# Performance work log

Hardware: AMD Instinct MI355X
Metric: run time of the kernel (lower is better)

Reference implementation:

```python
import jax, jax.numpy as jnp
import numpy as np

EPS = 1e-5

def _layernorm(x, g, b):
    m = jnp.mean(x, axis=-1, keepdims=True)
    v = jnp.mean((x - m) ** 2, axis=-1, keepdims=True)
    return (x - m) * jax.lax.rsqrt(v + EPS) * g + b

def setup_inputs() -> dict:
    key = jax.random.key(0)
    ks = jax.random.split(key, 16)
    B, N, L, E, D, NL = 1, 40962, 256, 4, 163848, 6
    inp = {}
    inp['mesh_latent'] = jax.random.normal(ks[0], (B, N, L), dtype=jnp.float32)
    inp['edge_index'] = jax.random.randint(ks[1], (2, D), 0, N, dtype=jnp.int32)
    inp['edge_attr'] = jax.random.normal(ks[2], (D, E), dtype=jnp.float32)
    s_e = 1.0 / np.sqrt(2 * L + E)
    s_n = 1.0 / np.sqrt(2 * L)
    s_o = 1.0 / np.sqrt(L)
    inp['We_w'] = jax.random.uniform(ks[3], (NL, 2 * L + E, L), jnp.float32, -s_e, s_e)
    inp['We_b'] = jax.random.uniform(ks[4], (NL, L), jnp.float32, -s_e, s_e)
    inp['ln1_g'] = jnp.ones((NL, L), jnp.float32)
    inp['ln1_b'] = jnp.zeros((NL, L), jnp.float32)
    inp['Wn1_w'] = jax.random.uniform(ks[5], (NL, 2 * L, L), jnp.float32, -s_n, s_n)
    inp['Wn1_b'] = jax.random.uniform(ks[6], (NL, L), jnp.float32, -s_n, s_n)
    inp['ln2_g'] = jnp.ones((NL, L), jnp.float32)
    inp['ln2_b'] = jnp.zeros((NL, L), jnp.float32)
    inp['Wn2_w'] = jax.random.uniform(ks[7], (NL, L, L), jnp.float32, -s_o, s_o)
    inp['Wn2_b'] = jax.random.uniform(ks[8], (NL, L), jnp.float32, -s_o, s_o)
    return inp

def reference(mesh_latent, edge_index, edge_attr, We_w, We_b, ln1_g, ln1_b,
              Wn1_w, Wn1_b, ln2_g, ln2_b, Wn2_w, Wn2_b):
    src = edge_index[0]  # x_j (source)
    dst = edge_index[1]  # x_i (target), also aggregation index
    N = mesh_latent.shape[1]
    L = mesh_latent.shape[2]
    # precompute edge_attr contribution is layer-dependent, done inside scan

    def layer(x, p):
        we_w, we_b, g1, b1, wn1_w, wn1_b, g2, b2, wn2_w, wn2_b = p
        x_i = x[dst]  # [E, L] target node feats
        x_j = x[src]  # [E, L] source node feats
        # edge MLP on cat([x_i, x_j, edge_attr]) without materializing the concat
        h = x_i @ we_w[:L] + x_j @ we_w[L:2 * L] + edge_attr @ we_w[2 * L:] + we_b
        msg = jax.nn.silu(_layernorm(h, g1, b1))  # [E, L]
        agg = jax.ops.segment_sum(msg, dst, num_segments=N)  # [N, L]
        u = x @ wn1_w[:L] + agg @ wn1_w[L:] + wn1_b
        u = jax.nn.silu(_layernorm(u, g2, b2)) @ wn2_w + wn2_b
        return x + u, None

    params = (We_w, We_b, ln1_g, ln1_b, Wn1_w, Wn1_b, ln2_g, ln2_b, Wn2_w, Wn2_b)

    def per_sample(x):
        x_out, _ = jax.lax.scan(layer, x, params)
        return x_out

    return jax.vmap(per_sample)(mesh_latent)
```

## Files before the change

### kernel.cpp

```cpp
#include <hip/hip_runtime.h>
#include <hip/hip_bf16.h>
#include <math.h>


#define NNODES 40962
#define NEDGES 163848
#define NLAYERS 6
#define MPAD 41088

typedef __attribute__((ext_vector_type(8))) short short8;
typedef __attribute__((ext_vector_type(4))) float f32x4;
typedef unsigned short ushort_t;

__device__ __forceinline__ void async_copy16(void* lds, const void* g) {
    __builtin_amdgcn_global_load_lds(
        (const __attribute__((address_space(1))) unsigned int*)g,
        (__attribute__((address_space(3))) unsigned int*)lds, 16, 0, 0);
}

__device__ __forceinline__ void bsplit(float v, ushort_t& h, ushort_t& l) {
    unsigned int u = __float_as_uint(v);
    h = (ushort_t)(u >> 16);
    float hf = __uint_as_float(u & 0xFFFF0000u);
    l = (ushort_t)(__float_as_uint(v - hf) >> 16);
}

__global__ __launch_bounds__(256) void wprep_kernel(
    const float* __restrict__ src, ushort_t* __restrict__ dst,
    int R, int C, size_t src_lstride, size_t src_hstride, int halves)
{
    __shared__ float t[32][33];
    const int b = blockIdx.z;
    src += (size_t)(b / halves) * src_lstride + (size_t)(b % halves) * src_hstride;
    dst += (size_t)b * R * C;
    const int tx = threadIdx.x & 31, ty = threadIdx.x >> 5;
    const int c0 = blockIdx.x * 32, r0 = blockIdx.y * 32;
    #pragma unroll
    for (int i = 0; i < 4; ++i)
        t[ty + 8 * i][tx] = src[(size_t)(r0 + ty + 8 * i) * C + c0 + tx];
    __syncthreads();
    #pragma unroll
    for (int i = 0; i < 4; ++i) {
        unsigned int u = __float_as_uint(t[tx][ty + 8 * i]);
        ushort_t h = (ushort_t)((u + 0x7FFFu + ((u >> 16) & 1u)) >> 16);
        dst[(size_t)(c0 + ty + 8 * i) * R + r0 + tx] = h;
    }
}

__global__ __launch_bounds__(256) void split_kernel(
    const float* __restrict__ x, ushort_t* __restrict__ xh,
    ushort_t* __restrict__ xl, int n4)
{
    int idx = blockIdx.x * 256 + threadIdx.x;
    if (idx >= n4) return;
    float4 v = ((const float4*)x)[idx];
    ushort4 oh, ol;
    bsplit(v.x, oh.x, ol.x); bsplit(v.y, oh.y, ol.y);
    bsplit(v.z, oh.z, ol.z); bsplit(v.w, oh.w, ol.w);
    ((ushort4*)xh)[idx] = oh;
    ((ushort4*)xl)[idx] = ol;
}

__global__ __launch_bounds__(256) void gemm_mfma(
    const ushort_t* __restrict__ A1h, const ushort_t* __restrict__ A1l,
    const ushort_t* __restrict__ A2h, const ushort_t* __restrict__ A2l,
    const ushort_t* __restrict__ BT,
    const float* __restrict__ bias, const float* __restrict__ resid,
    float* __restrict__ C, ushort_t* __restrict__ Ch, ushort_t* __restrict__ Cl,
    int M, int K, int ldC)
{
    __shared__ __align__(16) short AhS[128 * 32];
    __shared__ __align__(16) short AlS[128 * 32];
    __shared__ __align__(16) short BsS[128 * 32];

    const int tid = threadIdx.x;
    const int wave = tid >> 6;
    const int lane = tid & 63;
    const int m0 = blockIdx.x * 128;
    const int n0 = blockIdx.y * 128;
    const int wm = wave >> 1, wn = wave & 1;
    const int fm = lane & 15, quad = lane >> 4;

    const int rA = wave * 32 + (lane >> 2);
    const int qg = (lane & 3) ^ ((lane >> 3) & 3);
    const size_t offA = (size_t)(m0 + rA) * 256 + qg * 8;
    const size_t offB = (size_t)(n0 + rA) * (size_t)K + qg * 8;
    char* ldsAh = (char*)AhS + wave * 2048;
    char* ldsAl = (char*)AlS + wave * 2048;
    char* ldsB  = (char*)BsS + wave * 2048;

    const int sq16 = ((quad ^ ((fm >> 1) & 3)) << 4);

    f32x4 acc[4][4];
    #pragma unroll
    for (int i = 0; i < 4; ++i)
        #pragma unroll
        for (int j = 0; j < 4; ++j)
            acc[i][j] = (f32x4){0.f, 0.f, 0.f, 0.f};

    const int nkt = K >> 5;
    for (int kt = 0; kt < nkt; ++kt) {
        const int k0 = kt << 5;
        const ushort_t* Ah_g = A1h;
        const ushort_t* Al_g = A1l;
        int kb = k0;
        if (k0 >= 256) { Ah_g = A2h; Al_g = A2l; kb = k0 - 256; }

        async_copy16(ldsAh,        Ah_g + offA + kb);
        async_copy16(ldsAh + 1024, Ah_g + offA + 4096 + kb);
        async_copy16(ldsAl,        Al_g + offA + kb);
        async_copy16(ldsAl + 1024, Al_g + offA + 4096 + kb);
        async_copy16(ldsB,         BT + offB + k0);
        async_copy16(ldsB + 1024,  BT + offB + (size_t)16 * K + k0);

        __syncthreads();

        short8 afh[4], afl[4], bf[4];
        #pragma unroll
        for (int i = 0; i < 4; ++i) {
            const int r = wm * 64 + i * 16 + fm;
            afh[i] = *(const short8*)((const char*)AhS + (r << 6) + sq16);
            afl[i] = *(const short8*)((const char*)AlS + (r << 6) + sq16);
        }
        #pragma unroll
        for (int j = 0; j < 4; ++j) {
            const int r = wn * 64 + j * 16 + fm;
            bf[j] = *(const short8*)((const char*)BsS + (r << 6) + sq16);
        }
        #pragma unroll
        for (int i = 0; i < 4; ++i)
            #pragma unroll
            for (int j = 0; j < 4; ++j) {
                acc[i][j] = __builtin_amdgcn_mfma_f32_16x16x32_bf16(afl[i], bf[j], acc[i][j], 0, 0, 0);
                acc[i][j] = __builtin_amdgcn_mfma_f32_16x16x32_bf16(afh[i], bf[j], acc[i][j], 0, 0, 0);
            }

        __syncthreads();
    }

    #pragma unroll
    for (int j = 0; j < 4; ++j) {
        const int gc = n0 + wn * 64 + j * 16 + fm;
        const float bj = bias ? bias[gc] : 0.f;
        #pragma unroll
        for (int i = 0; i < 4; ++i) {
            #pragma unroll
            for (int r = 0; r < 4; ++r) {
                const int gr = m0 + wm * 64 + i * 16 + quad * 4 + r;
                if (gr < M) {
                    float v = acc[i][j][r] + bj;
                    if (resid) v += resid[(size_t)gr * ldC + gc];
                    C[(size_t)gr * ldC + gc] = v;
                    if (Ch) {
                        ushort_t hs, ls;
                        bsplit(v, hs, ls);
                        Ch[(size_t)gr * 256 + gc] = hs;
                        Cl[(size_t)gr * 256 + gc] = ls;
                    }
                }
            }
        }
    }
}

__device__ __forceinline__ float wave_sum(float v) {
    #pragma unroll
    for (int o = 32; o > 0; o >>= 1) v += __shfl_xor(v, o);
    return v;
}

__global__ __launch_bounds__(256) void count_kernel(
    const int* __restrict__ dst, int* __restrict__ deg, int E)
{
    int e = blockIdx.x * 256 + threadIdx.x;
    if (e < E) atomicAdd(&deg[dst[e]], 1);
}

__global__ __launch_bounds__(1024) void scan_kernel(
    const int* __restrict__ deg, int* __restrict__ rowptr, int n)
{
    __shared__ int wsum[16];
    __shared__ int carry_s;
    const int tid = threadIdx.x;
    const int lane = tid & 63, wave = tid >> 6;
    if (tid == 0) carry_s = 0;
    __syncthreads();

    for (int base = 0; base < n; base += 1024) {
        int i = base + tid;
        int v = (i < n) ? deg[i] : 0;
        int x = v;
        #pragma unroll
        for (int o = 1; o < 64; o <<= 1) {
            int t = __shfl_up(x, o);
            if (lane >= o) x += t;
        }
        if (lane == 63) wsum[wave] = x;
        __syncthreads();
        if (wave == 0 && lane < 16) {
            int w = wsum[lane];
            #pragma unroll
            for (int o = 1; o < 16; o <<= 1) {
                int t = __shfl_up(w, o);
                if (lane >= o) w += t;
            }
            wsum[lane] = w;
        }
        __syncthreads();
        int wave_off = (wave == 0) ? 0 : wsum[wave - 1];
        int incl = x + wave_off + carry_s;
        if (i < n) rowptr[i] = incl - v;
        __syncthreads();
        if (tid == 0) carry_s += wsum[15];
        __syncthreads();
    }
    if (tid == 0) rowptr[n] = carry_s;
}

__global__ __launch_bounds__(256) void scatter_kernel(
    const int* __restrict__ dst, int* __restrict__ cursor,
    int* __restrict__ esorted, int E)
{
    int e = blockIdx.x * 256 + threadIdx.x;
    if (e < E) {
        int p = atomicAdd(&cursor[dst[e]], 1);
        esorted[p] = e;
    }
}

__global__ __launch_bounds__(256) void node_agg_kernel(
    const float* __restrict__ P,
    const int* __restrict__ src,
    const float* __restrict__ attr,
    const float* __restrict__ W3,
    const float* __restrict__ be, const float* __restrict__ g1, const float* __restrict__ b1,
    const int* __restrict__ rowptr, const int* __restrict__ esorted,
    ushort_t* __restrict__ aggh, ushort_t* __restrict__ aggl, int N)
{
    const int wave = threadIdx.x >> 6;
    const int lane = threadIdx.x & 63;
    const int n = blockIdx.x * 4 + wave;
    if (n >= N) return;
    const int c0 = lane * 4;

    float4 p1 = *(const float4*)(P + (size_t)n * 512 + c0);
    const float* p1p = (const float*)&p1;

    float w30[4], w31[4], w32[4], w33[4], bev[4], g1v[4], b1v[4];
    #pragma unroll
    for (int i = 0; i < 4; ++i) {
        const int c = c0 + i;
        w30[i] = W3[c]; w31[i] = W3[256 + c]; w32[i] = W3[512 + c]; w33[i] = W3[768 + c];
        bev[i] = be[c]; g1v[i] = g1[c]; b1v[i] = b1[c];
    }

    float acc[4] = {0.f, 0.f, 0.f, 0.f};
    const int beg = rowptr[n];
    const int end = rowptr[n + 1];

    if (beg < end) {
        int iB0 = (beg + 1 < end) ? beg + 1 : beg;
        int eA = esorted[beg], eB = esorted[iB0];
        int sA = src[eA], sB = src[eB];
        float4 psA = *(const float4*)(P + (size_t)sA * 512 + 256 + c0);
        float4 avA = *(const float4*)(attr + (size_t)eA * 4);
        float4 psB = *(const float4*)(P + (size_t)sB * 512 + 256 + c0);
        float4 avB = *(const float4*)(attr + (size_t)eB * 4);
        bool vB = (beg + 1 < end);

        for (int i = beg; i < end; i += 2) {
            int jA = (i + 2 < end) ? i + 2 : i;
            int jB = (i + 3 < end) ? i + 3 : jA;
            int eA2 = esorted[jA], eB2 = esorted[jB];
            int sA2 = src[eA2], sB2 = src[eB2];
            float4 psA2 = *(const float4*)(P + (size_t)sA2 * 512 + 256 + c0);
            float4 avA2 = *(const float4*)(attr + (size_t)eA2 * 4);
            float4 psB2 = *(const float4*)(P + (size_t)sB2 * 512 + 256 + c0);
            float4 avB2 = *(const float4*)(attr + (size_t)eB2 * 4);

            const float* pA = (const float*)&psA;
            const float* pB = (const float*)&psB;
            float hA[4], hB[4];
            #pragma unroll
            for (int j = 0; j < 4; ++j) {
                float wA = avA.x * w30[j] + avA.y * w31[j] + avA.z * w32[j] + avA.w * w33[j];
                hA[j] = p1p[j] + pA[j] + wA + bev[j];
                float wB = avB.x * w30[j] + avB.y * w31[j] + avB.z * w32[j] + avB.w * w33[j];
                hB[j] = p1p[j] + pB[j] + wB + bev[j];
            }

            float s1A = hA[0] + hA[1] + hA[2] + hA[3];
            float s2A = hA[0]*hA[0] + hA[1]*hA[1] + hA[2]*hA[2] + hA[3]*hA[3];
            float s1B = hB[0] + hB[1] + hB[2] + hB[3];
            float s2B = hB[0]*hB[0] + hB[1]*hB[1] + hB[2]*hB[2] + hB[3]*hB[3];
            #pragma unroll
            for (int o = 32; o > 0; o >>= 1) {
                s1A += __shfl_xor(s1A, o); s2A += __shfl_xor(s2A, o);
                s1B += __shfl_xor(s1B, o); s2B += __shfl_xor(s2B, o);
            }
            const float mA = s1A * (1.0f / 256.0f);
            const float vrA = fmaxf(s2A * (1.0f / 256.0f) - mA * mA, 0.f);
            const float rA = rsqrtf(vrA + 1e-5f);
            const float mB = s1B * (1.0f / 256.0f);
            const float vrB = fmaxf(s2B * (1.0f / 256.0f) - mB * mB, 0.f);
            const float rB = rsqrtf(vrB + 1e-5f);
            const float addB = vB ? 1.f : 0.f;

            #pragma unroll
            for (int j = 0; j < 4; ++j) {
                float yA = (hA[j] - mA) * rA * g1v[j] + b1v[j];
                acc[j] += yA / (1.0f + __expf(-yA));
                float yB = (hB[j] - mB) * rB * g1v[j] + b1v[j];
                acc[j] += addB * (yB / (1.0f + __expf(-yB)));
            }

            psA = psA2; avA = avA2; psB = psB2; avB = avB2;
            vB = (i + 3 < end);
        }
    }

    ushort4 oh, ol;
    bsplit(acc[0], oh.x, ol.x); bsplit(acc[1], oh.y, ol.y);
    bsplit(acc[2], oh.z, ol.z); bsplit(acc[3], oh.w, ol.w);
    *(ushort4*)(aggh + (size_t)n * 256 + c0) = oh;
    *(ushort4*)(aggl + (size_t)n * 256 + c0) = ol;
}

__global__ __launch_bounds__(256) void ln_silu_kernel(
    const float* __restrict__ u, const float* __restrict__ g, const float* __restrict__ b,
    ushort_t* __restrict__ sh, ushort_t* __restrict__ sl, int N)
{
    const int wave = threadIdx.x >> 6;
    const int lane = threadIdx.x & 63;
    const int r = blockIdx.x * 4 + wave;
    if (r >= N) return;

    float4 hv = *(const float4*)(u + (size_t)r * 256 + lane * 4);
    float h[4] = {hv.x, hv.y, hv.z, hv.w};

    float s1 = h[0] + h[1] + h[2] + h[3];
    float s2 = h[0]*h[0] + h[1]*h[1] + h[2]*h[2] + h[3]*h[3];
    #pragma unroll
    for (int o = 32; o > 0; o >>= 1) {
        s1 += __shfl_xor(s1, o); s2 += __shfl_xor(s2, o);
    }
    const float mean = s1 * (1.0f / 256.0f);
    const float var = fmaxf(s2 * (1.0f / 256.0f) - mean * mean, 0.f);
    const float rstd = rsqrtf(var + 1e-5f);

    ushort4 oh, ol;
    #pragma unroll
    for (int i = 0; i < 4; ++i) {
        const int c = lane * 4 + i;
        float y = (h[i] - mean) * rstd * g[c] + b[c];
        h[i] = y / (1.0f + __expf(-y));
    }
    bsplit(h[0], oh.x, ol.x); bsplit(h[1], oh.y, ol.y);
    bsplit(h[2], oh.z, ol.z); bsplit(h[3], oh.w, ol.w);
    *(ushort4*)(sh + (size_t)r * 256 + lane * 4) = oh;
    *(ushort4*)(sl + (size_t)r * 256 + lane * 4) = ol;
}

extern "C" void kernel_launch(void* const* d_in, const int* in_sizes, int n_in,
                              void* d_out, int out_size, void* d_ws, size_t ws_size,
                              hipStream_t stream) {
    const float* mesh   = (const float*)d_in[0];
    const int*   eidx   = (const int*)  d_in[1];
    const float* eattr  = (const float*)d_in[2];
    const float* We_w   = (const float*)d_in[3];
    const float* We_b   = (const float*)d_in[4];
    const float* ln1_g  = (const float*)d_in[5];
    const float* ln1_b  = (const float*)d_in[6];
    const float* Wn1_w  = (const float*)d_in[7];
    const float* Wn1_b  = (const float*)d_in[8];
    const float* ln2_g  = (const float*)d_in[9];
    const float* ln2_b  = (const float*)d_in[10];
    const float* Wn2_w  = (const float*)d_in[11];
    const float* Wn2_b  = (const float*)d_in[12];

    const int N = NNODES, E = NEDGES;

    float* x = (float*)d_out;
    float* P = (float*)d_ws;
    float* u = P;
    int*   deg     = (int*)(P + (size_t)N * 512);
    int*   rowptr  = deg + N;
    int*   cursor  = rowptr + (N + 1);
    int*   esorted = cursor + N;
    uintptr_t wp = (uintptr_t)(esorted + E);
    wp = (wp + 63) & ~(uintptr_t)63;
    ushort_t* BTe  = (ushort_t*)wp;
    ushort_t* BTn1 = BTe  + (size_t)6 * 512 * 256;
    ushort_t* BTn2 = BTn1 + (size_t)6 * 256 * 512;
    ushort_t* xh   = BTn2 + (size_t)6 * 256 * 256;
    ushort_t* xl   = xh + (size_t)MPAD * 256;
    ushort_t* sh   = xl + (size_t)MPAD * 256;
    ushort_t* sl   = sh + (size_t)MPAD * 256;

    const int* src = eidx;
    const int* dst = eidx + E;

    hipMemcpyAsync(x, mesh, (size_t)N * 256 * sizeof(float),
                   hipMemcpyDeviceToDevice, stream);

    const size_t padoff = (size_t)N * 256;
    const size_t padbytes = (size_t)(MPAD - N) * 256 * sizeof(ushort_t);
    hipMemsetAsync(xh + padoff, 0, padbytes, stream);
    hipMemsetAsync(xl + padoff, 0, padbytes, stream);
    hipMemsetAsync(sh + padoff, 0, padbytes, stream);
    hipMemsetAsync(sl + padoff, 0, padbytes, stream);

    const int n4 = N * 64;
    split_kernel<<<(n4 + 255) / 256, 256, 0, stream>>>(mesh, xh, xl, n4);

    wprep_kernel<<<dim3(8, 8, 12), 256, 0, stream>>>(
        We_w, BTe, 256, 256, (size_t)516 * 256, (size_t)256 * 256, 2);
    wprep_kernel<<<dim3(8, 16, 6), 256, 0, stream>>>(
        Wn1_w, BTn1, 512, 256, (size_t)512 * 256, 0, 1);
    wprep_kernel<<<dim3(8, 8, 6), 256, 0, stream>>>(
        Wn2_w, BTn2, 256, 256, (size_t)256 * 256, 0, 1);

    hipMemsetAsync(deg, 0, (size_t)N * sizeof(int), stream);
    count_kernel<<<(E + 255) / 256, 256, 0, stream>>>(dst, deg, E);
    scan_kernel<<<1, 1024, 0, stream>>>(deg, rowptr, N);
    hipMemcpyAsync(cursor, rowptr, (size_t)N * sizeof(int),
                   hipMemcpyDeviceToDevice, stream);
    scatter_kernel<<<(E + 255) / 256, 256, 0, stream>>>(dst, cursor, esorted, E);

    const int mblocks = MPAD / 128;
    const int node_blocks = (N + 3) / 4;

    for (int l = 0; l < NLAYERS; ++l) {
        const float* W3  = We_w + (size_t)l * 516 * 256 + (size_t)512 * 256;
        const float* be  = We_b  + (size_t)l * 256;
        const float* g1  = ln1_g + (size_t)l * 256;
        const float* b1  = ln1_b + (size_t)l * 256;
        const float* bn1 = Wn1_b + (size_t)l * 256;
        const float* g2  = ln2_g + (size_t)l * 256;
        const float* b2  = ln2_b + (size_t)l * 256;
        const float* bn2 = Wn2_b + (size_t)l * 256;
        const ushort_t* bte  = BTe  + (size_t)l * 512 * 256;
        const ushort_t* btn1 = BTn1 + (size_t)l * 256 * 512;
        const ushort_t* btn2 = BTn2 + (size_t)l * 256 * 256;

        gemm_mfma<<<dim3(mblocks, 4), 256, 0, stream>>>(
            xh, xl, nullptr, nullptr, bte, nullptr, nullptr,
            P, nullptr, nullptr, N, 256, 512);
        node_agg_kernel<<<node_blocks, 256, 0, stream>>>(
            P, src, eattr, W3, be, g1, b1, rowptr, esorted, sh, sl, N);
        gemm_mfma<<<dim3(mblocks, 2), 256, 0, stream>>>(
            xh, xl, sh, sl, btn1, bn1, nullptr,
            u, nullptr, nullptr, N, 512, 256);
        ln_silu_kernel<<<node_blocks, 256, 0, stream>>>(u, g2, b2, sh, sl, N);
        gemm_mfma<<<dim3(mblocks, 2), 256, 0, stream>>>(
            sh, sl, nullptr, nullptr, btn2, bn2, x,
            x, (l < NLAYERS - 1) ? xh : nullptr, (l < NLAYERS - 1) ? xl : nullptr,
            N, 256, 256);
    }
}
```

Baseline: 1.791 ms.

## Double-buffer LDS tiles in MFMA GEMM to overlap loads with compute

Doubles the LDS buffers for the A-high, A-low and B tiles and issues the async global-to-LDS copies for the next K tile before computing on the current one. Each iteration now has a single barrier instead of two. The aim is to hide global load latency behind the MFMA work. LDS use per block doubles, which may reduce occupancy. The barrier placement may also not ensure the prefetched data has landed before it is read, since the async copy completion is not explicitly waited on.

```diff
diff --git a/kernel.cpp b/kernel.cpp
--- a/kernel.cpp
+++ b/kernel.cpp
@@ -69,9 +69,9 @@
     float* __restrict__ C, ushort_t* __restrict__ Ch, ushort_t* __restrict__ Cl,
     int M, int K, int ldC)
 {
-    __shared__ __align__(16) short AhS[128 * 32];
-    __shared__ __align__(16) short AlS[128 * 32];
-    __shared__ __align__(16) short BsS[128 * 32];
+    __shared__ __align__(16) short AhS[2 * 4096];
+    __shared__ __align__(16) short AlS[2 * 4096];
+    __shared__ __align__(16) short BsS[2 * 4096];
 
     const int tid = threadIdx.x;
     const int wave = tid >> 6;
@@ -85,9 +85,7 @@
     const int qg = (lane & 3) ^ ((lane >> 3) & 3);
     const size_t offA = (size_t)(m0 + rA) * 256 + qg * 8;
     const size_t offB = (size_t)(n0 + rA) * (size_t)K + qg * 8;
-    char* ldsAh = (char*)AhS + wave * 2048;
-    char* ldsAl = (char*)AlS + wave * 2048;
-    char* ldsB  = (char*)BsS + wave * 2048;
+    const int ldsoff = wave * 2048;
 
     const int sq16 = ((quad ^ ((fm >> 1) & 3)) << 4);
 
@@ -99,33 +97,46 @@
             acc[i][j] = (f32x4){0.f, 0.f, 0.f, 0.f};
 
     const int nkt = K >> 5;
-    for (int kt = 0; kt < nkt; ++kt) {
+
+    auto stage = [&](int kt, int bufsel) {
         const int k0 = kt << 5;
         const ushort_t* Ah_g = A1h;
         const ushort_t* Al_g = A1l;
         int kb = k0;
         if (k0 >= 256) { Ah_g = A2h; Al_g = A2l; kb = k0 - 256; }
-
-        async_copy16(ldsAh,        Ah_g + offA + kb);
-        async_copy16(ldsAh + 1024, Ah_g + offA + 4096 + kb);
-        async_copy16(ldsAl,        Al_g + offA + kb);
-        async_copy16(ldsAl + 1024, Al_g + offA + 4096 + kb);
-        async_copy16(ldsB,         BT + offB + k0);
-        async_copy16(ldsB + 1024,  BT + offB + (size_t)16 * K + k0);
-
-        __syncthreads();
+        char* dAh = (char*)AhS + bufsel * 8192 + ldsoff;
+        char* dAl = (char*)AlS + bufsel * 8192 + ldsoff;
+        char* dB  = (char*)BsS + bufsel * 8192 + ldsoff;
+        async_copy16(dAh,        Ah_g + offA + kb);
+        async_copy16(dAh + 1024, Ah_g + offA + 4096 + kb);
+        async_copy16(dAl,        Al_g + offA + kb);
+        async_copy16(dAl + 1024, Al_g + offA + 4096 + kb);
+        async_copy16(dB,         BT + offB + k0);
+        async_copy16(dB + 1024,  BT + offB + (size_t)16 * K + k0);
+    };
+
+    stage(0, 0);
+    __syncthreads();
+
+    int cur = 0;
+    for (int kt = 0; kt < nkt; ++kt) {
+        if (kt + 1 < nkt) stage(kt + 1, cur ^ 1);
+
+        const char* bAh = (const char*)AhS + cur * 8192;
+        const char* bAl = (const char*)AlS + cur * 8192;
+        const char* bB  = (const char*)BsS + cur * 8192;
 
         short8 afh[4], afl[4], bf[4];
         #pragma unroll
         for (int i = 0; i < 4; ++i) {
             const int r = wm * 64 + i * 16 + fm;
-            afh[i] = *(const short8*)((const char*)AhS + (r << 6) + sq16);
-            afl[i] = *(const short8*)((const char*)AlS + (r << 6) + sq16);
+            afh[i] = *(const short8*)(bAh + (r << 6) + sq16);
+            afl[i] = *(const short8*)(bAl + (r << 6) + sq16);
         }
         #pragma unroll
         for (int j = 0; j < 4; ++j) {
             const int r = wn * 64 + j * 16 + fm;
-            bf[j] = *(const short8*)((const char*)BsS + (r << 6) + sq16);
+            bf[j] = *(const short8*)(bB + (r << 6) + sq16);
         }
         #pragma unroll
         for (int i = 0; i < 4; ++i)
@@ -136,6 +147,7 @@
             }
 
         __syncthreads();
+        cur ^= 1;
     }
 
     #pragma unroll
```

New measurement: 1.777 ms. Within noise of the previous version (-0.8%).

## Load GEMM MFMA fragments directly from global memory instead of LDS staging

Applied to the files above, without the earlier changes.

Removes the LDS staging buffers, the async global-to-LDS copies and both barriers in the MFMA GEMM main loop. Each wave now reads its bf16 A-hi/A-lo and B fragments straight from global memory into registers. This drops synchronization and LDS traffic, but data is no longer shared across the two waves that use the same rows. That raises global/L2 traffic and leaves no explicit prefetch, so the loop may become latency bound.

```diff
diff --git a/kernel.cpp b/kernel.cpp
--- a/kernel.cpp
+++ b/kernel.cpp
@@ -11,12 +11,6 @@
 typedef __attribute__((ext_vector_type(8))) short short8;
 typedef __attribute__((ext_vector_type(4))) float f32x4;
 typedef unsigned short ushort_t;
-
-__device__ __forceinline__ void async_copy16(void* lds, const void* g) {
-    __builtin_amdgcn_global_load_lds(
-        (const __attribute__((address_space(1))) unsigned int*)g,
-        (__attribute__((address_space(3))) unsigned int*)lds, 16, 0, 0);
-}
 
 __device__ __forceinline__ void bsplit(float v, ushort_t& h, ushort_t& l) {
     unsigned int u = __float_as_uint(v);
@@ -69,10 +63,6 @@
     float* __restrict__ C, ushort_t* __restrict__ Ch, ushort_t* __restrict__ Cl,
     int M, int K, int ldC)
 {
-    __shared__ __align__(16) short AhS[128 * 32];
-    __shared__ __align__(16) short AlS[128 * 32];
-    __shared__ __align__(16) short BsS[128 * 32];
-
     const int tid = threadIdx.x;
     const int wave = tid >> 6;
     const int lane = tid & 63;
@@ -80,16 +70,15 @@
     const int n0 = blockIdx.y * 128;
     const int wm = wave >> 1, wn = wave & 1;
     const int fm = lane & 15, quad = lane >> 4;
-
-    const int rA = wave * 32 + (lane >> 2);
-    const int qg = (lane & 3) ^ ((lane >> 3) & 3);
-    const size_t offA = (size_t)(m0 + rA) * 256 + qg * 8;
-    const size_t offB = (size_t)(n0 + rA) * (size_t)K + qg * 8;
-    char* ldsAh = (char*)AhS + wave * 2048;
-    char* ldsAl = (char*)AlS + wave * 2048;
-    char* ldsB  = (char*)BsS + wave * 2048;
-
-    const int sq16 = ((quad ^ ((fm >> 1) & 3)) << 4);
+    const int ko = quad * 8;
+
+    size_t aOff[4], bOff[4];
+    #pragma unroll
+    for (int i = 0; i < 4; ++i)
+        aOff[i] = (size_t)(m0 + wm * 64 + i * 16 + fm) * 256 + ko;
+    #pragma unroll
+    for (int j = 0; j < 4; ++j)
+        bOff[j] = (size_t)(n0 + wn * 64 + j * 16 + fm) * (size_t)K + ko;
 
     f32x4 acc[4][4];
     #pragma unroll
@@ -106,27 +95,16 @@
         int kb = k0;
         if (k0 >= 256) { Ah_g = A2h; Al_g = A2l; kb = k0 - 256; }
 
-        async_copy16(ldsAh,        Ah_g + offA + kb);
-        async_copy16(ldsAh + 1024, Ah_g + offA + 4096 + kb);
-        async_copy16(ldsAl,        Al_g + offA + kb);
-        async_copy16(ldsAl + 1024, Al_g + offA + 4096 + kb);
-        async_copy16(ldsB,         BT + offB + k0);
-        async_copy16(ldsB + 1024,  BT + offB + (size_t)16 * K + k0);
-
-        __syncthreads();
-
         short8 afh[4], afl[4], bf[4];
         #pragma unroll
         for (int i = 0; i < 4; ++i) {
-            const int r = wm * 64 + i * 16 + fm;
-            afh[i] = *(const short8*)((const char*)AhS + (r << 6) + sq16);
-            afl[i] = *(const short8*)((const char*)AlS + (r << 6) + sq16);
+            afh[i] = *(const short8*)(Ah_g + aOff[i] + kb);
+            afl[i] = *(const short8*)(Al_g + aOff[i] + kb);
         }
         #pragma unroll
-        for (int j = 0; j < 4; ++j) {
-            const int r = wn * 64 + j * 16 + fm;
-            bf[j] = *(const short8*)((const char*)BsS + (r << 6) + sq16);
-        }
+        for (int j = 0; j < 4; ++j)
+            bf[j] = *(const short8*)(BT + bOff[j] + k0);
+
         #pragma unroll
         for (int i = 0; i < 4; ++i)
             #pragma unroll
@@ -134,8 +112,6 @@
                 acc[i][j] = __builtin_amdgcn_mfma_f32_16x16x32_bf16(afl[i], bf[j], acc[i][j], 0, 0, 0);
                 acc[i][j] = __builtin_amdgcn_mfma_f32_16x16x32_bf16(afh[i], bf[j], acc[i][j], 0, 0, 0);
             }
-
-        __syncthreads();
     }
 
     #pragma unroll
```

Measured after the change: 2.806 ms. 56.7% more time.
